# Kernel optimization log

Hardware: AMD Instinct MI355X
Metric: run time of the kernel (lower is better)

## Reference

```python
import jax, jax.numpy as jnp
import numpy as np

EPS = 1e-12
NUM_IDS = 25          # instance ids 0..24 (0 = background)
INTER_MARGIN = 0.2
W_SEM_ALIGN, W_SEM_MEM, W_INS_CON, W_INS_MEM = 0.5, 1.0, 1.0, 1.0


def _l2norm(x, axis):
    return x / jnp.maximum(jnp.linalg.norm(x, axis=axis, keepdims=True), EPS)


def _flat_pix(x):  # [B,T,C,H,W] -> [B*T*H*W, C]
    B, T, C, H, W = x.shape
    return jnp.transpose(x, (0, 1, 3, 4, 2)).reshape(B * T * H * W, C)


def _seg_ids(mask_r):  # [B,T,Hp,Wp] int -> [BT*N] global segment ids
    B, T, Hp, Wp = mask_r.shape
    bt = jnp.arange(B * T, dtype=jnp.int32)[:, None] * NUM_IDS
    return (mask_r.reshape(B * T, Hp * Wp) + bt).reshape(-1)


def _mask_nearest_half(inst_mask):
    # torch nearest interp H -> H/2 picks src index floor(i*2) = 2i
    return inst_mask[:, :, ::2, ::2]


def _gt_bilinear_half(x):
    B, T, C, H, W = x.shape
    return x.reshape(B, T, C, H // 2, 2, W // 2, 2).mean(axis=(4, 6))


def _sem_align_loss(refined_sem, lseg_gt, inst_mask):
    # fused replacement of the per-(b,t,instance) python loops: one segment-reduce pass
    B, T, C, Hp, Wp = refined_sem.shape
    mask_r = _mask_nearest_half(inst_mask)
    gt = _l2norm(_gt_bilinear_half(lseg_gt), axis=2)
    pred = _l2norm(refined_sem, axis=2)
    predf, gtf = _flat_pix(pred), _flat_pix(gt)
    seg = _seg_ids(mask_r)
    nseg = B * T * NUM_IDS
    sums = jax.ops.segment_sum(gtf, seg, num_segments=nseg)
    cnts = jax.ops.segment_sum(jnp.ones_like(seg, jnp.float32), seg, num_segments=nseg)
    # normalize(mean) == normalize(sum); prototype is detached in the original
    proto = jax.lax.stop_gradient(_l2norm(sums, axis=1))
    cos_loss = 1.0 - jnp.sum(predf * proto[seg], axis=1)
    valid = (mask_r.reshape(-1) > 0) & (cnts[seg] >= 2.0)
    total = jnp.sum(jnp.where(valid, cos_loss, 0.0))
    count = jnp.maximum(jnp.sum(valid.astype(jnp.float32)), 1.0)
    return total / count


def _memory_loss(pred_feat, mem_feat, mem_mask):
    pred = _l2norm(pred_feat, axis=2)
    tgt = jax.lax.stop_gradient(_l2norm(mem_feat, axis=2))
    cos_dist = (1.0 - jnp.sum(pred * tgt, axis=2, keepdims=True)) * mem_mask
    return jnp.sum(cos_dist) / jnp.maximum(jnp.sum(mem_mask), 1.0)


def _ins_contrastive_loss(refined_ins, inst_mask):
    # ContrastiveLoss(inter_mode='hinge', inter_margin=0.2, normalize_feats=True)
    B, T, C, Hp, Wp = refined_ins.shape
    mask_r = _mask_nearest_half(inst_mask)
    feat = _l2norm(refined_ins, axis=2)
    featf = _flat_pix(feat)
    seg = _seg_ids(mask_r)
    nseg = B * T * NUM_IDS
    sums = jax.ops.segment_sum(featf, seg, num_segments=nseg)
    cnts = jax.ops.segment_sum(jnp.ones_like(seg, jnp.float32), seg, num_segments=nseg)
    proto = _l2norm(sums, axis=1)  # [BT*K, C]
    # intra: pull pixels toward their instance prototype
    cos_loss = 1.0 - jnp.sum(featf * proto[seg], axis=1)
    valid = (mask_r.reshape(-1) > 0) & (cnts[seg] >= 2.0)
    intra = jnp.sum(jnp.where(valid, cos_loss, 0.0)) / jnp.maximum(
        jnp.sum(valid.astype(jnp.float32)), 1.0)
    # inter: hinge pushing apart prototypes of different instances within a scene
    P = proto.reshape(B * T, NUM_IDS, C)
    vmask = (cnts.reshape(B * T, NUM_IDS) >= 2.0) & (jnp.arange(NUM_IDS)[None, :] > 0)
    sim = jnp.einsum('bkc,blc->bkl', P, P)
    pair = vmask[:, :, None] & vmask[:, None, :] & ~jnp.eye(NUM_IDS, dtype=bool)[None]
    hinge = jnp.maximum(sim - INTER_MARGIN, 0.0)
    inter = jnp.sum(jnp.where(pair, hinge, 0.0)) / jnp.maximum(
        jnp.sum(pair.astype(jnp.float32)), 1.0)
    return intra + inter


def setup_inputs() -> dict:
    key = jax.random.key(0)
    ks = jax.random.split(key, 7)
    B, T, C_SEM, C_INS, HP, WP = 2, 4, 512, 64, 64, 64
    H, W = 2 * HP, 2 * WP
    return {
        "refined_sem": jax.random.normal(ks[0], (B, T, C_SEM, HP, WP), jnp.float32),
        "refined_ins": jax.random.normal(ks[1], (B, T, C_INS, HP, WP), jnp.float32),
        "lseg_gt": jax.random.normal(ks[2], (B, T, C_SEM, H, W), jnp.float32),
        "mem_sem": jax.random.normal(ks[3], (B, T, C_SEM, HP, WP), jnp.float32),
        "mem_ins": jax.random.normal(ks[4], (B, T, C_INS, HP, WP), jnp.float32),
        "mem_mask": (jax.random.uniform(ks[5], (B, T, 1, HP, WP)) < 0.7).astype(jnp.float32),
        "inst_mask": jax.random.randint(ks[6], (B, T, H, W), 0, NUM_IDS, dtype=jnp.int32),
    }


def reference(refined_sem, refined_ins, lseg_gt, mem_sem, mem_ins, mem_mask, inst_mask):
    sem_align = _sem_align_loss(refined_sem, lseg_gt, inst_mask)
    sem_mem = _memory_loss(refined_sem, mem_sem, mem_mask)
    ins_con = _ins_contrastive_loss(refined_ins, inst_mask)
    ins_mem = _memory_loss(refined_ins, mem_ins, mem_mask)
    objective = (W_SEM_ALIGN * sem_align + W_SEM_MEM * sem_mem
                 + W_INS_CON * ins_con + W_INS_MEM * ins_mem)
    return objective
```

## Files before the change

### kernel.cpp

```cpp
#include <hip/hip_runtime.h>

typedef unsigned short u16;
typedef unsigned int u32;
typedef unsigned long long u64;

#define NID 25


#define SC16  65536.0f
#define ISC16 (1.0f/65536.0f)
#define SC32  4294967296.0f

__device__ __forceinline__ float bf2f(u16 h){ return __uint_as_float(((u32)h) << 16); }
__device__ __forceinline__ u16 f2bf(float f){
  u32 u = __float_as_uint(f);
  u32 r = u + 0x7fffu + ((u >> 16) & 1u);
  return (u16)(r >> 16);
}

template<bool BF>
__device__ __forceinline__ float LD(const void* p, size_t i){
  if constexpr (BF) return bf2f(((const u16*)p)[i]);
  else return ((const float*)p)[i];
}
template<bool BF>
__device__ __forceinline__ float2 LD2(const void* p, size_t i){
  if constexpr (BF){
    ushort2 v = *(const ushort2*)((const u16*)p + i);
    return make_float2(bf2f(v.x), bf2f(v.y));
  } else {
    return *(const float2*)((const float*)p + i);
  }
}

__global__ __launch_bounds__(256) void k_probe(const u32* __restrict__ x,
                                               int* __restrict__ flag){
  __shared__ int cnt;
  if (threadIdx.x == 0) cnt = 0;
  __syncthreads();
  int c = 0;
  for (int i = threadIdx.x; i < 1024; i += 256){
    u32 e = (x[i] >> 7) & 0xffu;
    c += (e >= 100 && e <= 140) ? 1 : 0;
  }
  atomicAdd(&cnt, c);
  __syncthreads();
  if (threadIdx.x == 0) *flag = (cnt >= 600) ? 1 : 0;
}

template<bool BF>
__device__ void p1_body(const void* lg, const int* __restrict__ im,
                        int* __restrict__ sem_sums, int* __restrict__ cnts){
  __shared__ int   sums[8*25*65];
  __shared__ float pp[8*64];
  __shared__ float invl[64];
  __shared__ int   hist[NID];
  const int t = threadIdx.x, g = t >> 6, q = t & 63;
  const int bt = blockIdx.y;
  const int hr0 = blockIdx.x * 4;

  for (int k = t; k < 8*25*65; k += 512) sums[k] = 0;
  if (t < NID) hist[t] = 0;
  __syncthreads();

  for (int r = 0; r < 4; ++r){
    const int hr = hr0 + r;
    u32 mr[32];
    float ps = 0.f;
    #pragma unroll 8
    for (int cc = 0; cc < 64; ++cc){
      const int c = g*64 + cc;
      const size_t o = ((size_t)(bt*512 + c) << 14) + (hr << 8) + (q << 1);
      float2 a = LD2<BF>(lg, o);
      float2 b = LD2<BF>(lg, o + 128);
      float m = (a.x + a.y + b.x + b.y) * 0.25f;
      ps += m*m;
      u16 mb = f2bf(m);
      if (cc & 1) mr[cc>>1] |= ((u32)mb << 16);
      else        mr[cc>>1]  = (u32)mb;
    }
    pp[g*64 + q] = ps;
    __syncthreads();
    if (t < 64){
      float s = 0.f;
      #pragma unroll
      for (int k = 0; k < 8; ++k) s += pp[k*64 + t];
      invl[t] = SC16 / fmaxf(sqrtf(s), 1e-12f);
    }
    __syncthreads();
    const int id = im[(bt << 14) + (hr << 8) + (q << 1)];
    if (g == 0) atomicAdd(&hist[id], 1);
    const float inv = invl[q];
    int* dst = &sums[g*1625 + id*65];
    #pragma unroll 8
    for (int cc = 0; cc < 64; ++cc){
      u16 mb = (cc & 1) ? (u16)(mr[cc>>1] >> 16) : (u16)(mr[cc>>1] & 0xffffu);
      atomicAdd(&dst[cc], (int)rintf(bf2f(mb) * inv));
    }
    __syncthreads();
  }

  for (int k = t; k < 25*512; k += 512){
    const int id2 = k >> 9, c2 = k & 511, g2 = c2 >> 6, cc2 = c2 & 63;
    const int v = sums[g2*1625 + id2*65 + cc2];
    if (v) atomicAdd(&sem_sums[(bt*NID + id2)*512 + c2], v);
  }
  if (t < NID && hist[t] > 0) atomicAdd(&cnts[bt*NID + t], hist[t]);
}
__global__ __launch_bounds__(512) void k_p1(const void* lg, const int* im,
    int* sem_sums, int* cnts, const int* flag){
  if (*flag) p1_body<true>(lg, im, sem_sums, cnts);
  else       p1_body<false>(lg, im, sem_sums, cnts);
}

template<bool BF>
__device__ void p4_body(const void* ri, const int* __restrict__ im,
                        int* __restrict__ ins_sums){
  __shared__ int   sums[2*25*33];
  __shared__ float parts[2][128];
  const int t = threadIdx.x;
  const int pb = blockIdx.x * 128;
  const int bt = pb >> 12;
  const int h = t >> 7, q = t & 127;
  const int p = (pb + q) & 4095;
  const int id = im[(bt << 14) + ((p >> 6) << 8) + ((p & 63) << 1)];
  for (int k = t; k < 2*25*33; k += 256) sums[k] = 0;
  float vals[32];
  float ffh = 0.f;
  #pragma unroll
  for (int cc = 0; cc < 32; ++cc){
    float v = LD<BF>(ri, (size_t)(bt*64 + h*32 + cc)*4096 + p);
    vals[cc] = v; ffh += v*v;
  }
  parts[h][q] = ffh;
  __syncthreads();
  const float inv = SC16 / fmaxf(sqrtf(parts[0][q] + parts[1][q]), 1e-12f);
  int* dst = &sums[h*825 + id*33];
  #pragma unroll
  for (int cc = 0; cc < 32; ++cc) atomicAdd(&dst[cc], (int)rintf(vals[cc]*inv));
  __syncthreads();
  for (int k = t; k < 1600; k += 256){
    const int id2 = k >> 6, c2 = k & 63, h2 = c2 >> 5, cc2 = c2 & 31;
    const int v = sums[h2*825 + id2*33 + cc2];
    if (v) atomicAdd(&ins_sums[(bt*NID + id2)*64 + c2], v);
  }
}
__global__ __launch_bounds__(256) void k_p4(const void* ri, const int* im,
    int* ins_sums, const int* flag){
  if (*flag) p4_body<true>(ri, im, ins_sums);
  else       p4_body<false>(ri, im, ins_sums);
}

__global__ __launch_bounds__(256) void k_p5(const int* __restrict__ sem_sums,
    const int* __restrict__ ins_sums, const int* __restrict__ cnts,
    float* __restrict__ proto_sem, float* __restrict__ proto_ins,
    int* __restrict__ valid_tab){
  const int wg = blockIdx.x*4 + (threadIdx.x >> 6);
  const int l  = threadIdx.x & 63;
  if (blockIdx.x < 50){
    const int seg = wg;
    float v[8]; float ss = 0.f;
    const size_t base = (size_t)seg*512 + l;
    #pragma unroll
    for (int k = 0; k < 8; ++k){
      v[k] = (float)sem_sums[base + 64*k] * ISC16;
      ss += v[k]*v[k];
    }
    for (int m = 1; m < 64; m <<= 1) ss += __shfl_xor(ss, m, 64);
    const float inv = 1.f / fmaxf(sqrtf(ss), 1e-12f);
    #pragma unroll
    for (int k = 0; k < 8; ++k) proto_sem[base + 64*k] = v[k]*inv;
    if (l == 0) valid_tab[seg] = (cnts[seg] >= 2 && (seg % NID) != 0) ? 1 : 0;
  } else {
    const int seg = wg - 200;
    float v = (float)ins_sums[(size_t)seg*64 + l] * ISC16;
    float ss = v*v;
    for (int m = 1; m < 64; m <<= 1) ss += __shfl_xor(ss, m, 64);
    proto_ins[(size_t)seg*64 + l] = v * (1.f / fmaxf(sqrtf(ss), 1e-12f));
  }
}

template<bool BF>
__device__ void p3_body(const void* rs, const void* ms, const void* mmask,
    const int* __restrict__ im, const float* __restrict__ proto_sem,
    const int* __restrict__ valid_tab, u64* __restrict__ sc){
  __shared__ float protoT[25*513];
  __shared__ float4 parts[3][64];
  __shared__ int vt[NID];
  const int t = threadIdx.x;
  const int pb = blockIdx.x * 64;
  const int bt = pb >> 12;
  const int w = t >> 6, q = t & 63;
  const int g = pb + q, p = g & 4095;
  for (int f = t; f < 12800; f += 256){
    const int id2 = f >> 9, c2 = f & 511;
    protoT[id2*513 + c2] = proto_sem[(size_t)(bt*NID + id2)*512 + c2];
  }
  if (t < NID) vt[t] = valid_tab[bt*NID + t];
  __syncthreads();
  const int id = im[(bt << 14) + ((p >> 6) << 8) + ((p & 63) << 1)];
  const size_t cbase = (size_t)(bt*512 + w*128)*4096 + p;
  const float* pr = &protoT[id*513 + w*128];
  float ppn = 0.f, pm = 0.f, mm = 0.f, pd = 0.f;
  #pragma unroll 8
  for (int cc = 0; cc < 128; ++cc){
    float pv = LD<BF>(rs, cbase + (size_t)cc*4096);
    float mv = LD<BF>(ms, cbase + (size_t)cc*4096);
    float pz = pr[cc];
    ppn += pv*pv; mm += mv*mv; pm += pv*mv; pd += pv*pz;
  }
  if (w > 0) parts[w-1][q] = make_float4(ppn, pm, mm, pd);
  __syncthreads();
  if (w == 0){
    #pragma unroll
    for (int k = 0; k < 3; ++k){
      float4 f4 = parts[k][q];
      ppn += f4.x; pm += f4.y; mm += f4.z; pd += f4.w;
    }
    const float npn = fmaxf(sqrtf(ppn), 1e-12f);
    const int vld = vt[id];
    float a_i = vld ? (1.f - pd/npn) : 0.f;
    float vc  = vld ? 1.f : 0.f;
    float mkv = LD<BF>(mmask, g);
    const float nmn = fmaxf(sqrtf(mm), 1e-12f);
    float s_i = mkv * (1.f - pm/(npn*nmn));
    for (int m = 1; m < 64; m <<= 1){
      a_i += __shfl_xor(a_i, m, 64);
      vc  += __shfl_xor(vc,  m, 64);
      s_i += __shfl_xor(s_i, m, 64);
      mkv += __shfl_xor(mkv, m, 64);
    }
    if (q == 0){
      long long v0 = llrintf(a_i * SC32);
      long long v2 = llrintf(s_i * SC32);
      if (v0) atomicAdd(&sc[0], (u64)v0);
      if (vc != 0.f) atomicAdd(&sc[1], (u64)llrintf(vc));
      if (v2) atomicAdd(&sc[2], (u64)v2);
      if (mkv != 0.f) atomicAdd(&sc[3], (u64)llrintf(mkv));
    }
  }
}
__global__ __launch_bounds__(256) void k_p3(const void* rs, const void* ms,
    const void* mmask, const int* im, const float* proto_sem,
    const int* valid_tab, u64* sc, const int* flag){
  if (*flag) p3_body<true>(rs, ms, mmask, im, proto_sem, valid_tab, sc);
  else       p3_body<false>(rs, ms, mmask, im, proto_sem, valid_tab, sc);
}

template<bool BF>
__device__ void p6_body(const void* ri, const void* mi, const void* mmask,
    const int* __restrict__ im, const float* __restrict__ proto_ins,
    const int* __restrict__ valid_tab, u64* __restrict__ sc){
  __shared__ float protoT[25*65];
  __shared__ float4 parts[128];
  __shared__ int vt[NID];
  const int t = threadIdx.x;
  const int pb = blockIdx.x * 128;
  const int bt = pb >> 12;
  const int h = t >> 7, q = t & 127;
  const int g = pb + q, p = g & 4095;
  for (int f = t; f < 1600; f += 256){
    const int id2 = f >> 6, c2 = f & 63;
    protoT[id2*65 + c2] = proto_ins[(size_t)(bt*NID + id2)*64 + c2];
  }
  if (t < NID) vt[t] = valid_tab[bt*NID + t];
  __syncthreads();
  const int id = im[(bt << 14) + ((p >> 6) << 8) + ((p & 63) << 1)];
  const size_t cbase = (size_t)(bt*64 + h*32)*4096 + p;
  const float* pr = &protoT[id*65 + h*32];
  float ff = 0.f, fm = 0.f, m2 = 0.f, fd = 0.f;
  #pragma unroll
  for (int cc = 0; cc < 32; ++cc){
    float fv = LD<BF>(ri, cbase + (size_t)cc*4096);
    float mv = LD<BF>(mi, cbase + (size_t)cc*4096);
    float pz = pr[cc];
    ff += fv*fv; m2 += mv*mv; fm += fv*mv; fd += fv*pz;
  }
  if (h == 1) parts[q] = make_float4(ff, fm, m2, fd);
  __syncthreads();
  if (h == 0){
    float4 f4 = parts[q];
    ff += f4.x; fm += f4.y; m2 += f4.z; fd += f4.w;
    const float nf = fmaxf(sqrtf(ff), 1e-12f);
    float ii = vt[id] ? (1.f - fd/nf) : 0.f;
    const float mkv = LD<BF>(mmask, g);
    const float nm = fmaxf(sqrtf(m2), 1e-12f);
    float mi_ = mkv * (1.f - fm/(nf*nm));
    for (int m = 1; m < 64; m <<= 1){
      ii  += __shfl_xor(ii,  m, 64);
      mi_ += __shfl_xor(mi_, m, 64);
    }
    if ((t & 63) == 0){
      long long v4 = llrintf(ii  * SC32);
      long long v5 = llrintf(mi_ * SC32);
      if (v4) atomicAdd(&sc[4], (u64)v4);
      if (v5) atomicAdd(&sc[5], (u64)v5);
    }
  }
}
__global__ __launch_bounds__(256) void k_p6(const void* ri, const void* mi,
    const void* mmask, const int* im, const float* proto_ins,
    const int* valid_tab, u64* sc, const int* flag){
  if (*flag) p6_body<true>(ri, mi, mmask, im, proto_ins, valid_tab, sc);
  else       p6_body<false>(ri, mi, mmask, im, proto_ins, valid_tab, sc);
}

__global__ __launch_bounds__(256) void k_f(const float* __restrict__ proto_ins,
    const int* __restrict__ valid_tab, const u64* __restrict__ sc,
    u32* __restrict__ out){
  __shared__ float P[25*65];
  __shared__ int vt[NID];
  __shared__ float red[8];
  const int t = threadIdx.x;
  float hsum = 0.f, pcnt = 0.f;
  for (int bt = 0; bt < 8; ++bt){
    __syncthreads();
    for (int f = t; f < 1600; f += 256){
      const int id2 = f >> 6, c2 = f & 63;
      P[id2*65 + c2] = proto_ins[bt*1600 + f];
    }
    if (t < NID) vt[t] = valid_tab[bt*NID + t];
    __syncthreads();
    for (int kl = t; kl < 625; kl += 256){
      const int k = kl / 25, l = kl - k*25;
      if (k != l && vt[k] && vt[l]){
        float s = 0.f;
        #pragma unroll
        for (int c = 0; c < 64; ++c) s += P[k*65 + c] * P[l*65 + c];
        hsum += fmaxf(s - 0.2f, 0.f);
        pcnt += 1.f;
      }
    }
  }
  for (int m = 1; m < 64; m <<= 1){
    hsum += __shfl_xor(hsum, m, 64);
    pcnt += __shfl_xor(pcnt, m, 64);
  }
  __syncthreads();
  if ((t & 63) == 0){ red[t >> 6] = hsum; red[4 + (t >> 6)] = pcnt; }
  __syncthreads();
  if (t == 0){
    const float inter = red[0]+red[1]+red[2]+red[3];
    const float pc    = red[4]+red[5]+red[6]+red[7];
    const double S = 1.0 / 4294967296.0;
    const double asum = (double)(long long)sc[0] * S;
    const double vcnt = (double)(long long)sc[1];
    const double ssum = (double)(long long)sc[2] * S;
    const double mcnt = (double)(long long)sc[3];
    const double isum = (double)(long long)sc[4] * S;
    const double msum = (double)(long long)sc[5] * S;
    const double align = asum / (vcnt > 1.0 ? vcnt : 1.0);
    const double smem  = ssum / (mcnt > 1.0 ? mcnt : 1.0);
    const double intra = isum / (vcnt > 1.0 ? vcnt : 1.0);
    const double imem  = msum / (mcnt > 1.0 ? mcnt : 1.0);
    const double obj = 0.5*align + smem + intra + (double)(inter / fmaxf(pc, 1.f)) + imem;
    const u32 b = (u32)f2bf((float)obj);
    out[0] = (b << 16) | b;
  }
}

extern "C" void kernel_launch(void* const* d_in, const int* in_sizes, int n_in,
                              void* d_out, int out_size, void* d_ws, size_t ws_size,
                              hipStream_t stream){
  const void* rs    = d_in[0];
  const void* ri    = d_in[1];
  const void* lg    = d_in[2];
  const void* ms    = d_in[3];
  const void* mi    = d_in[4];
  const void* mmask = d_in[5];
  const int*  im    = (const int*)d_in[6];

  char* ws = (char*)d_ws;
  u64*   sc        = (u64*)  ws;
  int*   flag      = (int*)  (ws + 64);
  int*   cnts      = (int*)  (ws + 256);
  int*   sem_sums  = (int*)  (ws + 4096);
  int*   ins_sums  = (int*)  (ws + 413696);
  float* proto_sem = (float*)(ws + 466944);
  float* proto_ins = (float*)(ws + 876544);
  int*   valid_tab = (int*)  (ws + 927744);

  hipMemsetAsync(d_ws, 0, 464896, stream);
  k_probe<<<1, 256, 0, stream>>>((const u32*)rs, flag);
  k_p1<<<dim3(16, 8), 512, 0, stream>>>(lg, im, sem_sums, cnts, flag);
  k_p4<<<256, 256, 0, stream>>>(ri, im, ins_sums, flag);
  k_p5<<<100, 256, 0, stream>>>(sem_sums, ins_sums, cnts, proto_sem, proto_ins, valid_tab);
  k_p3<<<512, 256, 0, stream>>>(rs, ms, mmask, im, proto_sem, valid_tab, sc, flag);
  k_p6<<<256, 256, 0, stream>>>(ri, mi, mmask, im, proto_ins, valid_tab, sc, flag);
  k_f<<<1, 256, 0, stream>>>(proto_ins, valid_tab, sc, (u32*)d_out);
}
```

Measured before the change: 647.9 us.

## Split semantic prototype pass into norm and accumulate kernels; widen p3/p6 loads

The single p1 kernel, which ran only 128 blocks, becomes two kernels. A highly parallel p1a computes per-pixel squared norms of the downsampled lseg_gt into a fixed-point buffer. p1b then re-reads lseg_gt and accumulates normalized segment sums using 256 blocks. p3 and p6 now process two pixels per thread with vectorized float2 loads and split channels across more warps. The intent is better occupancy and memory-level parallelism, at the cost of reading lseg_gt twice and adding a fixed-point norm step. The ss buffer overlaps proto_sem in the workspace, which is acceptable only because p5 writes proto_sem after p1b has consumed ss.

```diff
diff --git a/kernel.cpp b/kernel.cpp
--- a/kernel.cpp
+++ b/kernel.cpp
@@ -9,6 +9,8 @@
 
 #define SC16  65536.0f
 #define ISC16 (1.0f/65536.0f)
+#define SC20  1048576.0f
+#define ISC20 (1.0f/1048576.0f)
 #define SC32  4294967296.0f
 
 __device__ __forceinline__ float bf2f(u16 h){ return __uint_as_float(((u32)h) << 16); }
@@ -32,6 +34,15 @@
     return *(const float2*)((const float*)p + i);
   }
 }
+template<bool BF>
+__device__ __forceinline__ float4 LD4(const void* p, size_t i){
+  if constexpr (BF){
+    ushort4 v = *(const ushort4*)((const u16*)p + i);
+    return make_float4(bf2f(v.x), bf2f(v.y), bf2f(v.z), bf2f(v.w));
+  } else {
+    return *(const float4*)((const float*)p + i);
+  }
+}
 
 __global__ __launch_bounds__(256) void k_probe(const u32* __restrict__ x,
                                                int* __restrict__ flag){
@@ -49,68 +60,87 @@
 }
 
 template<bool BF>
-__device__ void p1_body(const void* lg, const int* __restrict__ im,
-                        int* __restrict__ sem_sums, int* __restrict__ cnts){
-  __shared__ int   sums[8*25*65];
-  __shared__ float pp[8*64];
-  __shared__ float invl[64];
-  __shared__ int   hist[NID];
-  const int t = threadIdx.x, g = t >> 6, q = t & 63;
+__device__ void p1a_body(const void* lg, int* __restrict__ ss){
+  __shared__ int ps[64];
+  const int t = threadIdx.x;
+  const int hr = blockIdx.x;
+  const int cg = blockIdx.y;
+  const int bt = blockIdx.z;
+  const int q2 = t & 31;
+  const int cw = t >> 5;
+  if (t < 64) ps[t] = 0;
+  __syncthreads();
+  float s0 = 0.f, s1 = 0.f;
+  const int c0 = cg*64 + cw*8;
+  #pragma unroll
+  for (int k = 0; k < 8; ++k){
+    const size_t o = ((size_t)(bt*512 + c0 + k) << 14) + (hr << 8) + (q2 << 2);
+    float4 a = LD4<BF>(lg, o);
+    float4 b = LD4<BF>(lg, o + 128);
+    const float m0 = (a.x + a.y + b.x + b.y) * 0.25f;
+    const float m1 = (a.z + a.w + b.z + b.w) * 0.25f;
+    s0 += m0*m0; s1 += m1*m1;
+  }
+  atomicAdd(&ps[q2*2],     (int)rintf(s0 * SC20));
+  atomicAdd(&ps[q2*2 + 1], (int)rintf(s1 * SC20));
+  __syncthreads();
+  if (t < 64){
+    const int v = ps[t];
+    if (v) atomicAdd(&ss[(bt << 12) + (hr << 6) + t], v);
+  }
+}
+__global__ __launch_bounds__(256) void k_p1a(const void* lg, int* ss,
+                                             const int* flag){
+  if (*flag) p1a_body<true>(lg, ss);
+  else       p1a_body<false>(lg, ss);
+}
+
+template<bool BF>
+__device__ void p1b_body(const void* lg, const int* __restrict__ im,
+                         const int* __restrict__ ss,
+                         int* __restrict__ sem_sums, int* __restrict__ cnts){
+  __shared__ int sums[4*25*129];
+  __shared__ float invl[128];
+  __shared__ int hist[NID];
+  const int t = threadIdx.x;
   const int bt = blockIdx.y;
-  const int hr0 = blockIdx.x * 4;
-
-  for (int k = t; k < 8*25*65; k += 512) sums[k] = 0;
+  const int pxb = blockIdx.x * 128;
+  const int q = t & 127;
+  const int cw = t >> 7;
+  for (int k = t; k < 4*25*129; k += 512) sums[k] = 0;
   if (t < NID) hist[t] = 0;
-  __syncthreads();
-
-  for (int r = 0; r < 4; ++r){
-    const int hr = hr0 + r;
-    u32 mr[32];
-    float ps = 0.f;
-    #pragma unroll 8
-    for (int cc = 0; cc < 64; ++cc){
-      const int c = g*64 + cc;
-      const size_t o = ((size_t)(bt*512 + c) << 14) + (hr << 8) + (q << 1);
-      float2 a = LD2<BF>(lg, o);
-      float2 b = LD2<BF>(lg, o + 128);
-      float m = (a.x + a.y + b.x + b.y) * 0.25f;
-      ps += m*m;
-      u16 mb = f2bf(m);
-      if (cc & 1) mr[cc>>1] |= ((u32)mb << 16);
-      else        mr[cc>>1]  = (u32)mb;
-    }
-    pp[g*64 + q] = ps;
-    __syncthreads();
-    if (t < 64){
-      float s = 0.f;
-      #pragma unroll
-      for (int k = 0; k < 8; ++k) s += pp[k*64 + t];
-      invl[t] = SC16 / fmaxf(sqrtf(s), 1e-12f);
-    }
-    __syncthreads();
-    const int id = im[(bt << 14) + (hr << 8) + (q << 1)];
-    if (g == 0) atomicAdd(&hist[id], 1);
-    const float inv = invl[q];
-    int* dst = &sums[g*1625 + id*65];
-    #pragma unroll 8
-    for (int cc = 0; cc < 64; ++cc){
-      u16 mb = (cc & 1) ? (u16)(mr[cc>>1] >> 16) : (u16)(mr[cc>>1] & 0xffffu);
-      atomicAdd(&dst[cc], (int)rintf(bf2f(mb) * inv));
-    }
-    __syncthreads();
-  }
-
+  const int p = pxb + q;
+  const int id = im[(bt << 14) + ((p >> 6) << 8) + ((p & 63) << 1)];
+  if (t < 128){
+    const float sf = (float)ss[(bt << 12) + pxb + t] * ISC20;
+    invl[t] = SC16 / fmaxf(sqrtf(sf), 1e-12f);
+  }
+  __syncthreads();
+  if (t < 128) atomicAdd(&hist[id], 1);
+  const float inv = invl[q];
+  const size_t pbase = ((size_t)(bt*512 + cw*128) << 14)
+                     + ((p >> 6) << 8) + ((p & 63) << 1);
+  int* dst = &sums[(cw*25 + id)*129];
+  #pragma unroll 8
+  for (int k = 0; k < 128; ++k){
+    const size_t o = pbase + ((size_t)k << 14);
+    float2 a = LD2<BF>(lg, o);
+    float2 b = LD2<BF>(lg, o + 128);
+    const float m = (a.x + a.y + b.x + b.y) * 0.25f;
+    atomicAdd(&dst[k], (int)rintf(m * inv));
+  }
+  __syncthreads();
   for (int k = t; k < 25*512; k += 512){
-    const int id2 = k >> 9, c2 = k & 511, g2 = c2 >> 6, cc2 = c2 & 63;
-    const int v = sums[g2*1625 + id2*65 + cc2];
+    const int id2 = k >> 9, c2 = k & 511, cw2 = c2 >> 7, k2 = c2 & 127;
+    const int v = sums[(cw2*25 + id2)*129 + k2];
     if (v) atomicAdd(&sem_sums[(bt*NID + id2)*512 + c2], v);
   }
   if (t < NID && hist[t] > 0) atomicAdd(&cnts[bt*NID + t], hist[t]);
 }
-__global__ __launch_bounds__(512) void k_p1(const void* lg, const int* im,
-    int* sem_sums, int* cnts, const int* flag){
-  if (*flag) p1_body<true>(lg, im, sem_sums, cnts);
-  else       p1_body<false>(lg, im, sem_sums, cnts);
+__global__ __launch_bounds__(512) void k_p1b(const void* lg, const int* im,
+    const int* ss, int* sem_sums, int* cnts, const int* flag){
+  if (*flag) p1b_body<true>(lg, im, ss, sem_sums, cnts);
+  else       p1b_body<false>(lg, im, ss, sem_sums, cnts);
 }
 
 template<bool BF>
@@ -185,38 +215,49 @@
     const int* __restrict__ im, const float* __restrict__ proto_sem,
     const int* __restrict__ valid_tab, u64* __restrict__ sc){
   __shared__ float protoT[25*513];
-  __shared__ float4 parts[3][64];
+  __shared__ float4 parts[8][64];
   __shared__ int vt[NID];
   const int t = threadIdx.x;
   const int pb = blockIdx.x * 64;
   const int bt = pb >> 12;
-  const int w = t >> 6, q = t & 63;
-  const int g = pb + q, p = g & 4095;
+  const int w  = t >> 5;
+  const int l2 = t & 31;
   for (int f = t; f < 12800; f += 256){
     const int id2 = f >> 9, c2 = f & 511;
     protoT[id2*513 + c2] = proto_sem[(size_t)(bt*NID + id2)*512 + c2];
   }
   if (t < NID) vt[t] = valid_tab[bt*NID + t];
   __syncthreads();
-  const int id = im[(bt << 14) + ((p >> 6) << 8) + ((p & 63) << 1)];
-  const size_t cbase = (size_t)(bt*512 + w*128)*4096 + p;
-  const float* pr = &protoT[id*513 + w*128];
-  float ppn = 0.f, pm = 0.f, mm = 0.f, pd = 0.f;
+  const int p0 = (pb & 4095) + 2*l2;
+  const int p1 = p0 + 1;
+  const int id0 = im[(bt << 14) + ((p0 >> 6) << 8) + ((p0 & 63) << 1)];
+  const int id1 = im[(bt << 14) + ((p1 >> 6) << 8) + ((p1 & 63) << 1)];
+  const size_t cbase = (size_t)(bt*512 + w*64)*4096 + p0;
+  const float* pr0 = &protoT[id0*513 + w*64];
+  const float* pr1 = &protoT[id1*513 + w*64];
+  float pp0=0.f,pp1=0.f,pm0=0.f,pm1=0.f,mm0=0.f,mm1=0.f,pd0=0.f,pd1=0.f;
   #pragma unroll 8
-  for (int cc = 0; cc < 128; ++cc){
-    float pv = LD<BF>(rs, cbase + (size_t)cc*4096);
-    float mv = LD<BF>(ms, cbase + (size_t)cc*4096);
-    float pz = pr[cc];
-    ppn += pv*pv; mm += mv*mv; pm += pv*mv; pd += pv*pz;
-  }
-  if (w > 0) parts[w-1][q] = make_float4(ppn, pm, mm, pd);
-  __syncthreads();
-  if (w == 0){
+  for (int cc = 0; cc < 64; ++cc){
+    float2 pv = LD2<BF>(rs, cbase + (size_t)cc*4096);
+    float2 mv = LD2<BF>(ms, cbase + (size_t)cc*4096);
+    pp0 += pv.x*pv.x; pp1 += pv.y*pv.y;
+    mm0 += mv.x*mv.x; mm1 += mv.y*mv.y;
+    pm0 += pv.x*mv.x; pm1 += pv.y*mv.y;
+    pd0 += pv.x*pr0[cc]; pd1 += pv.y*pr1[cc];
+  }
+  parts[w][2*l2]   = make_float4(pp0, pm0, mm0, pd0);
+  parts[w][2*l2+1] = make_float4(pp1, pm1, mm1, pd1);
+  __syncthreads();
+  if (t < 64){
+    float ppn=0.f, pm=0.f, mm=0.f, pd=0.f;
     #pragma unroll
-    for (int k = 0; k < 3; ++k){
-      float4 f4 = parts[k][q];
+    for (int k = 0; k < 8; ++k){
+      float4 f4 = parts[k][t];
       ppn += f4.x; pm += f4.y; mm += f4.z; pd += f4.w;
     }
+    const int g = pb + t;
+    const int p = g & 4095;
+    const int id = im[(bt << 14) + ((p >> 6) << 8) + ((p & 63) << 1)];
     const float npn = fmaxf(sqrtf(ppn), 1e-12f);
     const int vld = vt[id];
     float a_i = vld ? (1.f - pd/npn) : 0.f;
@@ -230,7 +271,7 @@
       s_i += __shfl_xor(s_i, m, 64);
       mkv += __shfl_xor(mkv, m, 64);
     }
-    if (q == 0){
+    if (t == 0){
       long long v0 = llrintf(a_i * SC32);
       long long v2 = llrintf(s_i * SC32);
       if (v0) atomicAdd(&sc[0], (u64)v0);
@@ -252,35 +293,49 @@
     const int* __restrict__ im, const float* __restrict__ proto_ins,
     const int* __restrict__ valid_tab, u64* __restrict__ sc){
   __shared__ float protoT[25*65];
-  __shared__ float4 parts[128];
+  __shared__ float4 parts[4][128];
   __shared__ int vt[NID];
   const int t = threadIdx.x;
   const int pb = blockIdx.x * 128;
   const int bt = pb >> 12;
-  const int h = t >> 7, q = t & 127;
-  const int g = pb + q, p = g & 4095;
+  const int h2 = t >> 6;
+  const int q2 = t & 63;
   for (int f = t; f < 1600; f += 256){
     const int id2 = f >> 6, c2 = f & 63;
     protoT[id2*65 + c2] = proto_ins[(size_t)(bt*NID + id2)*64 + c2];
   }
   if (t < NID) vt[t] = valid_tab[bt*NID + t];
   __syncthreads();
-  const int id = im[(bt << 14) + ((p >> 6) << 8) + ((p & 63) << 1)];
-  const size_t cbase = (size_t)(bt*64 + h*32)*4096 + p;
-  const float* pr = &protoT[id*65 + h*32];
-  float ff = 0.f, fm = 0.f, m2 = 0.f, fd = 0.f;
+  const int p0 = (pb & 4095) + 2*q2;
+  const int p1 = p0 + 1;
+  const int id0 = im[(bt << 14) + ((p0 >> 6) << 8) + ((p0 & 63) << 1)];
+  const int id1 = im[(bt << 14) + ((p1 >> 6) << 8) + ((p1 & 63) << 1)];
+  const size_t cbase = (size_t)(bt*64 + h2*16)*4096 + p0;
+  const float* pr0 = &protoT[id0*65 + h2*16];
+  const float* pr1 = &protoT[id1*65 + h2*16];
+  float ff0=0.f,ff1=0.f,fm0=0.f,fm1=0.f,m20=0.f,m21=0.f,fd0=0.f,fd1=0.f;
   #pragma unroll
-  for (int cc = 0; cc < 32; ++cc){
-    float fv = LD<BF>(ri, cbase + (size_t)cc*4096);
-    float mv = LD<BF>(mi, cbase + (size_t)cc*4096);
-    float pz = pr[cc];
-    ff += fv*fv; m2 += mv*mv; fm += fv*mv; fd += fv*pz;
-  }
-  if (h == 1) parts[q] = make_float4(ff, fm, m2, fd);
-  __syncthreads();
-  if (h == 0){
-    float4 f4 = parts[q];
-    ff += f4.x; fm += f4.y; m2 += f4.z; fd += f4.w;
+  for (int cc = 0; cc < 16; ++cc){
+    float2 fv = LD2<BF>(ri, cbase + (size_t)cc*4096);
+    float2 mv = LD2<BF>(mi, cbase + (size_t)cc*4096);
+    ff0 += fv.x*fv.x; ff1 += fv.y*fv.y;
+    m20 += mv.x*mv.x; m21 += mv.y*mv.y;
+    fm0 += fv.x*mv.x; fm1 += fv.y*mv.y;
+    fd0 += fv.x*pr0[cc]; fd1 += fv.y*pr1[cc];
+  }
+  parts[h2][2*q2]   = make_float4(ff0, fm0, m20, fd0);
+  parts[h2][2*q2+1] = make_float4(ff1, fm1, m21, fd1);
+  __syncthreads();
+  if (t < 128){
+    float ff=0.f, fm=0.f, m2=0.f, fd=0.f;
+    #pragma unroll
+    for (int k = 0; k < 4; ++k){
+      float4 f4 = parts[k][t];
+      ff += f4.x; fm += f4.y; m2 += f4.z; fd += f4.w;
+    }
+    const int g = pb + t;
+    const int p = g & 4095;
+    const int id = im[(bt << 14) + ((p >> 6) << 8) + ((p & 63) << 1)];
     const float nf = fmaxf(sqrtf(ff), 1e-12f);
     float ii = vt[id] ? (1.f - fd/nf) : 0.f;
     const float mkv = LD<BF>(mmask, g);
@@ -376,13 +431,15 @@
   int*   cnts      = (int*)  (ws + 256);
   int*   sem_sums  = (int*)  (ws + 4096);
   int*   ins_sums  = (int*)  (ws + 413696);
+  int*   ss        = (int*)  (ws + 466944);
   float* proto_sem = (float*)(ws + 466944);
   float* proto_ins = (float*)(ws + 876544);
   int*   valid_tab = (int*)  (ws + 927744);
 
-  hipMemsetAsync(d_ws, 0, 464896, stream);
+  hipMemsetAsync(d_ws, 0, 598016, stream);
   k_probe<<<1, 256, 0, stream>>>((const u32*)rs, flag);
-  k_p1<<<dim3(16, 8), 512, 0, stream>>>(lg, im, sem_sums, cnts, flag);
+  k_p1a<<<dim3(64, 8, 8), 256, 0, stream>>>(lg, ss, flag);
+  k_p1b<<<dim3(32, 8), 512, 0, stream>>>(lg, im, ss, sem_sums, cnts, flag);
   k_p4<<<256, 256, 0, stream>>>(ri, im, ins_sums, flag);
   k_p5<<<100, 256, 0, stream>>>(sem_sums, ins_sums, cnts, proto_sem, proto_ins, valid_tab);
   k_p3<<<512, 256, 0, stream>>>(rs, ms, mmask, im, proto_sem, valid_tab, sc, flag);
```

Result: faster. 579.3 us (-10.6%).
